# Kernel tuning notes

Measured on AMD Instinct MI355X. Metric: run time of the kernel, lower is better.

The kernel has to match this reference:

```python
import jax, jax.numpy as jnp
import numpy as np
from jax import lax

B, C, T, H, W = 1, 64, 16, 48, 48
RC = C // 16

def conv2d(x, w, b=None, stride=1, pad=1):
    out = lax.conv_general_dilated(x, w, (stride, stride), [(pad, pad), (pad, pad)],
                                   dimension_numbers=('NCHW', 'OIHW', 'NCHW'))
    return out if b is None else out + b[None, :, None, None]

def dwconv3d(x, w, b, pad, dil):
    out = lax.conv_general_dilated(x, w, (1, 1, 1), [(p, p) for p in pad], rhs_dilation=dil,
                                   dimension_numbers=('NCDHW', 'OIDHW', 'NCDHW'),
                                   feature_group_count=x.shape[1])
    return out + b[None, :, None, None, None]

def grid_sample_zeros(img, grid):
    # img [N,Cc,Hh,Ww], grid [N,Hg,Wg,2] with (x,y) in [-1,1]; bilinear, zeros padding, align_corners=False
    N, Cc, Hh, Ww = img.shape
    gx, gy = grid[..., 0], grid[..., 1]
    x = ((gx + 1.0) * Ww - 1.0) * 0.5
    y = ((gy + 1.0) * Hh - 1.0) * 0.5
    x0 = jnp.floor(x); y0 = jnp.floor(y)
    imgf = img.reshape(N, Cc, Hh * Ww)
    def corner(xi, yi, wgt):
        valid = (xi >= 0) & (xi < Ww) & (yi >= 0) & (yi < Hh)
        idx = (jnp.clip(yi, 0, Hh - 1) * Ww + jnp.clip(xi, 0, Ww - 1)).astype(jnp.int32)
        vals = jnp.take_along_axis(imgf, idx.reshape(N, 1, -1), axis=2).reshape(N, Cc, *xi.shape[1:])
        return vals * (wgt * valid)[:, None]
    return (corner(x0, y0, (x0 + 1 - x) * (y0 + 1 - y)) + corner(x0 + 1, y0, (x - x0) * (y0 + 1 - y))
            + corner(x0, y0 + 1, (x0 + 1 - x) * (y - y0)) + corner(x0 + 1, y0 + 1, (x - x0) * (y - y0)))

def corr_attn(a, w1, w2):
    avg = jnp.mean(a, axis=1, keepdims=True)
    mx = jnp.max(a, axis=1, keepdims=True)
    var = jnp.var(a, axis=1, keepdims=True, ddof=1)  # torch unbiased var
    y = jax.nn.sigmoid(conv2d(jnp.concatenate([avg, mx], axis=1), w1, pad=1) + conv2d(var, w2, pad=1))
    return a * y

def setup_inputs() -> dict:
    key = jax.random.key(0)
    ks = jax.random.split(key, 16)
    def n(k, shape, s=0.05):
        return jax.random.normal(k, shape, jnp.float32) * s
    return {
        'x': jax.random.normal(ks[0], (B, C, T, H, W), jnp.float32),
        'w_dc2': n(ks[1], (C, C)),
        'w_ofs_l': n(ks[2], (2, C, 3, 3)), 'b_ofs_l': n(ks[3], (2,)),
        'w_ofs_r': n(ks[4], (2, C, 3, 3)), 'b_ofs_r': n(ks[5], (2,)),
        'ca_w1': n(ks[6], (1, 2, 3, 3)), 'ca_w2': n(ks[7], (1, 1, 3, 3)),
        'w_down': n(ks[8], (RC, C)),
        'sa1_w': n(ks[9], (RC, 1, 9, 3, 3)), 'sa1_b': n(ks[10], (RC,)),
        'sa2_w': n(ks[11], (RC, 1, 9, 3, 3)), 'sa2_b': n(ks[12], (RC,)),
        'sa3_w': n(ks[13], (RC, 1, 9, 3, 3)), 'sa3_b': n(ks[14], (RC,)),
        'weights': jnp.ones(3, jnp.float32) / 3,
        'weights2': jnp.ones(2, jnp.float32) / 2,
        'w_back': n(ks[15], (C, RC)),
    }

def reference(x, w_dc2, w_ofs_l, b_ofs_l, w_ofs_r, b_ofs_r, ca_w1, ca_w2, w_down,
              sa1_w, sa1_b, sa2_w, sa2_b, sa3_w, sa3_b, weights, weights2, w_back):
    Bq, Cq, Tq, Hq, Wq = x.shape
    x2 = jnp.einsum('oc,bcthw->bothw', w_dc2, x)  # 1x1x1 conv3d
    left_move = jnp.concatenate([x2[:, :, 1:], x2[:, :, -1:]], axis=2)
    right_move = jnp.concatenate([x2[:, :, :1], x2[:, :, :-1]], axis=2)
    to2d = lambda t: t.transpose(0, 2, 1, 3, 4).reshape(Bq * Tq, Cq, Hq, Wq)
    off_l = conv2d(to2d(x + left_move), w_ofs_l, b_ofs_l, stride=2, pad=1)  # [BT,2,H2,W2]
    off_r = conv2d(to2d(x + right_move), w_ofs_r, b_ofs_r, stride=2, pad=1)
    H2, W2 = off_l.shape[-2:]
    gx, gy = jnp.meshgrid(jnp.arange(W2, dtype=x.dtype), jnp.arange(H2, dtype=x.dtype), indexing='xy')
    base = jnp.stack([gx, gy]) * 2.0  # [2,H2,W2]; matches create_grid_like * 2
    def norm_grid(v):  # faithful to normalize_grid (ch0 scaled by H2-1, ch1 by W2-1)
        gh = 2.0 * v[:, 0] / max(H2 - 1, 1) - 1.0
        gw = 2.0 * v[:, 1] / max(W2 - 1, 1) - 1.0
        return jnp.stack([gh, gw], axis=-1)
    left_part = grid_sample_zeros(to2d(left_move), norm_grid(base[None] + off_l))
    right_part = grid_sample_zeros(to2d(right_move), norm_grid(base[None] + off_r))
    to5d = lambda t: t.reshape(Bq, Tq, Cq, H2, W2).transpose(0, 2, 1, 3, 4)  # [B,C,T,H2,W2]
    left_part = to5d(left_part); right_part = to5d(right_part)
    def branch(part, wscale):
        aff = jnp.einsum('bcthw,bctsd->bthwsd', x, part)  # all-pairs correlation volume
        a = aff.reshape(Bq * Tq, Hq, Wq, H2 * W2).transpose(0, 3, 1, 2)
        a = corr_attn(a, ca_w1, ca_w2)
        a = a.reshape(Bq, Tq, H2, W2, Hq, Wq).transpose(0, 1, 4, 5, 2, 3)  # [B,T,H,W,H2,W2]
        return jnp.einsum('bctsd,bthwsd->bcthw', part, jax.nn.sigmoid(a) - 0.5) * wscale
    features = branch(left_part, weights2[0]) + branch(right_part, weights2[1])
    xd = jnp.einsum('oc,bcthw->bothw', w_down, x)  # channel reduction
    agg = (dwconv3d(xd, sa1_w, sa1_b, (4, 1, 1), (1, 1, 1)) * weights[0]
           + dwconv3d(xd, sa2_w, sa2_b, (4, 2, 2), (1, 2, 2)) * weights[1]
           + dwconv3d(xd, sa3_w, sa3_b, (4, 3, 3), (1, 3, 3)) * weights[2])
    agg = jnp.einsum('oc,bcthw->bothw', w_back, agg)
    return features * (jax.nn.sigmoid(agg) - 0.5)
```

## Files before the change

### kernel.cpp

```cpp
#include <hip/hip_runtime.h>
#include <hip/hip_bf16.h>

#define T_    16
#define C_    64
#define H_    48
#define W_    48
#define HW_   2304
#define THW_  36864
#define CTHW_ 2359296
#define H2_   24
#define W2_   24
#define SD_   576
#define RC_   4
#define SDT_  72

typedef _Float16 half8 __attribute__((ext_vector_type(8)));
typedef _Float16 half4 __attribute__((ext_vector_type(4)));
typedef float f32x4 __attribute__((ext_vector_type(4)));

__device__ __forceinline__ float sigm(float v) {
    return __builtin_amdgcn_rcpf(1.f + __expf(-v));
}
__device__ __forceinline__ void soft_barrier() {
    asm volatile("s_waitcnt lgkmcnt(0)" ::: "memory");
    __builtin_amdgcn_s_barrier();
}

__global__ __launch_bounds__(256) void k_pre(const float* __restrict__ x,
                                             const float* __restrict__ w,
                                             const float* __restrict__ w_down,
                                             float* __restrict__ x2T,
                                             _Float16* __restrict__ xfh,
                                             float* __restrict__ xd) {
    int base = blockIdx.x * 64;
    __shared__ float wl[64 * 65];
    __shared__ float xt[4096];
    __shared__ float ld[64 * 65];
    __shared__ float wd[256];
    int tid = threadIdx.x;
    for (int i = tid; i < 4096; i += 256) wl[(i >> 6) * 65 + (i & 63)] = w[i];
    for (int i = tid; i < 4096; i += 256) {
        float v = x[(size_t)(i >> 6) * THW_ + base + (i & 63)];
        xt[i] = v;
        ld[(i >> 6) * 65 + (i & 63)] = v;
    }
    if (tid < 256) wd[tid] = w_down[tid];
    __syncthreads();
    {
        int o_grp = tid >> 4, u_grp = tid & 15;
        float acc[4][4] = {};
        const float4* xt4 = (const float4*)xt;
        for (int c = 0; c < 64; ++c) {
            float xa[4];
            *(float4*)xa = xt4[c * 16 + u_grp];
            #pragma unroll
            for (int i = 0; i < 4; ++i) {
                float wv = wl[(o_grp * 4 + i) * 65 + c];
                #pragma unroll
                for (int g = 0; g < 4; ++g) acc[i][g] += wv * xa[g];
            }
        }
        #pragma unroll
        for (int g = 0; g < 4; ++g) {
            float4 v = make_float4(acc[0][g], acc[1][g], acc[2][g], acc[3][g]);
            *(float4*)&x2T[(size_t)(base + u_grp * 4 + g) * 64 + o_grp * 4] = v;
        }
    }
    {
        int r = tid >> 6, u = tid & 63;
        float a = 0.f;
        #pragma unroll 8
        for (int c = 0; c < 64; ++c) a += wd[r * 64 + c] * xt[c * 64 + u];
        xd[(size_t)r * THW_ + base + u] = a;
    }
    for (int i = tid; i < 4096; i += 256) {
        int u = i >> 6, c = i & 63;
        xfh[(size_t)(base + u) * 64 + c] = (_Float16)ld[c * 65 + u];
    }
}

__global__ __launch_bounds__(256) void k_gs(const _Float16* __restrict__ xfh,
                                            const float* __restrict__ x2T,
                                            const float* __restrict__ w_l,
                                            const float* __restrict__ b_l,
                                            const float* __restrict__ w_r,
                                            const float* __restrict__ b_r,
                                            _Float16* __restrict__ pxh) {
    __shared__ float wlds[2304];
    int tid = threadIdx.x;
    for (int i = tid; i < 2304; i += 256) wlds[i] = (i < 1152) ? w_l[i] : w_r[i - 1152];
    __syncthreads();
    int wg = blockIdx.x * 4 + (tid >> 6);
    int lane = tid & 63;
    int sd = wg % 576;
    int t = (wg / 576) % 16;
    int side = wg / 9216;
    int j = sd % W2_, i = sd / W2_;
    int ts = (side == 0) ? min(t + 1, T_ - 1) : max(t - 1, 0);
    const float* wp = wlds + side * 1152;
    const _Float16* xhb = xfh + ((size_t)t * HW_) * 64 + lane;
    const float* x2l = x2T + (size_t)ts * HW_ * 64 + lane;
    float a0 = 0.f, a1 = 0.f;
    for (int ki = 0; ki < 3; ++ki) {
        int hh = 2 * i - 1 + ki;
        if (hh < 0 || hh >= H_) continue;
        for (int kj = 0; kj < 3; ++kj) {
            int ww = 2 * j - 1 + kj;
            if (ww < 0 || ww >= W_) continue;
            int pos = hh * W_ + ww;
            float s = (float)xhb[(size_t)pos * 64] + x2l[(size_t)pos * 64];
            int tap = ki * 3 + kj;
            a0 += s * wp[lane * 9 + tap];
            a1 += s * wp[576 + lane * 9 + tap];
        }
    }
    #pragma unroll
    for (int m = 32; m >= 1; m >>= 1) {
        a0 += __shfl_xor(a0, m);
        a1 += __shfl_xor(a1, m);
    }
    const float* bb = (side == 0) ? b_l : b_r;
    float v0 = 2.f * (float)j + (a0 + bb[0]);
    float v1 = 2.f * (float)i + (a1 + bb[1]);
    float xf = 48.f * v0 / 23.f - 0.5f;
    float yf = 48.f * v1 / 23.f - 0.5f;
    float x0 = floorf(xf), y0 = floorf(yf);
    int ix0 = (int)x0, iy0 = (int)y0;
    float fx = xf - x0, fy = yf - y0;
    float w00 = (1.f - fx) * (1.f - fy), w10 = fx * (1.f - fy);
    float w01 = (1.f - fx) * fy,         w11 = fx * fy;
    bool vx0 = (ix0 >= 0 && ix0 < W_), vx1 = (ix0 + 1 >= 0 && ix0 + 1 < W_);
    bool vy0 = (iy0 >= 0 && iy0 < H_), vy1 = (iy0 + 1 >= 0 && iy0 + 1 < H_);
    int cx0 = min(max(ix0, 0), W_ - 1), cx1 = min(max(ix0 + 1, 0), W_ - 1);
    int cy0 = min(max(iy0, 0), H_ - 1), cy1 = min(max(iy0 + 1, 0), H_ - 1);
    float m00 = (vx0 && vy0) ? w00 : 0.f;
    float m10 = (vx1 && vy0) ? w10 : 0.f;
    float m01 = (vx0 && vy1) ? w01 : 0.f;
    float m11 = (vx1 && vy1) ? w11 : 0.f;
    const float* img = x2T + (size_t)ts * HW_ * 64;
    float val = m00 * img[(size_t)(cy0 * W_ + cx0) * 64 + lane]
              + m10 * img[(size_t)(cy0 * W_ + cx1) * 64 + lane]
              + m01 * img[(size_t)(cy1 * W_ + cx0) * 64 + lane]
              + m11 * img[(size_t)(cy1 * W_ + cx1) * 64 + lane];
    size_t idx = ((size_t)(side * 16 + t) * 576 + sd) * 64 + lane;
    pxh[idx] = (_Float16)val;
}

__global__ __launch_bounds__(256) void k_stats(const _Float16* __restrict__ xfh,
                                               const _Float16* __restrict__ pxh,
                                               float* __restrict__ stats) {
    int bid = blockIdx.x;
    int side = bid & 1;
    int tb = bid >> 1;
    int t = tb / 36, hwt = tb % 36;
    int base = t * HW_ + hwt * 64;
    __shared__ __attribute__((aligned(16))) _Float16 ps[2][64 * SDT_];
    int tid = threadIdx.x;
    int lane = tid & 63, wv = tid >> 6;
    int quad = lane >> 4, l15 = lane & 15;
    int m0 = wv * 16;
    const _Float16* xr = xfh + (size_t)(base + m0 + l15) * 64;
    half8 a0 = *(const half8*)&xr[quad * 8];
    half8 a1 = *(const half8*)&xr[32 + quad * 8];
    int sH[4], sC[4];
    #pragma unroll
    for (int k = 0; k < 4; ++k) { int i = tid + k * 256; sH[k] = i >> 4; sC[k] = i & 15; }
    const _Float16* phb = pxh + (size_t)(side * 16 + t) * 576 * 64;
    uint2 pf[4];
    #pragma unroll
    for (int k = 0; k < 4; ++k)
        pf[k] = *(const uint2*)&phb[(size_t)sH[k] * 64 + sC[k] * 4];
    float sum[4] = {}, sq[4] = {};
    float mx[4] = {-1e30f, -1e30f, -1e30f, -1e30f};
    for (int kt = 0; kt < 9; ++kt) {
        int b = kt & 1;
        #pragma unroll
        for (int k = 0; k < 4; ++k)
            *(uint2*)&ps[b][sH[k] * SDT_ + sC[k] * 4] = pf[k];
        if (kt < 8) {
            const _Float16* ph = phb + (size_t)(kt + 1) * 4096;
            #pragma unroll
            for (int k = 0; k < 4; ++k)
                pf[k] = *(const uint2*)&ph[(size_t)sH[k] * 64 + sC[k] * 4];
        }
        soft_barrier();
        #pragma unroll
        for (int tile = 0; tile < 4; ++tile) {
            half8 b0 = *(const half8*)&ps[b][(tile * 16 + l15) * SDT_ + quad * 8];
            half8 b1 = *(const half8*)&ps[b][(tile * 16 + l15) * SDT_ + 32 + quad * 8];
            f32x4 dacc = {0.f, 0.f, 0.f, 0.f};
            dacc = __builtin_amdgcn_mfma_f32_16x16x32_f16(a0, b0, dacc, 0, 0, 0);
            dacc = __builtin_amdgcn_mfma_f32_16x16x32_f16(a1, b1, dacc, 0, 0, 0);
            #pragma unroll
            for (int r = 0; r < 4; ++r) {
                float v = dacc[r];
                sum[r] += v; sq[r] += v * v; mx[r] = fmaxf(mx[r], v);
            }
        }
    }
    #pragma unroll
    for (int m = 1; m < 16; m <<= 1)
        #pragma unroll
        for (int r = 0; r < 4; ++r) {
            sum[r] += __shfl_xor(sum[r], m);
            sq[r]  += __shfl_xor(sq[r], m);
            mx[r]   = fmaxf(mx[r], __shfl_xor(mx[r], m));
        }
    if (l15 == 0) {
        #pragma unroll
        for (int r = 0; r < 4; ++r) {
            int thw = base + m0 + quad * 4 + r;
            stats[(side * 3 + 0) * THW_ + thw] = sum[r] * (1.f / 576.f);
            stats[(side * 3 + 1) * THW_ + thw] = mx[r];
            stats[(side * 3 + 2) * THW_ + thw] =
                (sq[r] - sum[r] * sum[r] * (1.f / 576.f)) * (1.f / 575.f);
        }
    }
}

__global__ __launch_bounds__(256) void k_aux(const float* __restrict__ stats,
                      const float* __restrict__ ca_w1,
                      const float* __restrict__ ca_w2, float* __restrict__ yb,
                      const float* __restrict__ xd,
                      const float* __restrict__ w1, const float* __restrict__ b1,
                      const float* __restrict__ w2, const float* __restrict__ b2,
                      const float* __restrict__ w3, const float* __restrict__ b3,
                      const float* __restrict__ wts, float* __restrict__ agg0,
                      const _Float16* __restrict__ pxh,
                      _Float16* __restrict__ partb) {
    __shared__ unsigned short ld[64 * 68];
    int blk = blockIdx.x;
    int tid = threadIdx.x;
    if (blk < (2 * THW_) / 256) {
        int idx = blk * 256 + tid;
        int side = idx / THW_, thw = idx % THW_;
        int w = thw % W_, h = (thw / W_) % H_, t = thw / HW_;
        const float* avg = stats + (side * 3 + 0) * THW_ + t * HW_;
        const float* mxp = stats + (side * 3 + 1) * THW_ + t * HW_;
        const float* var = stats + (side * 3 + 2) * THW_ + t * HW_;
        float acc = 0.f;
        for (int ki = 0; ki < 3; ++ki) {
            int hh = h - 1 + ki;
            if (hh < 0 || hh >= H_) continue;
            for (int kj = 0; kj < 3; ++kj) {
                int ww = w - 1 + kj;
                if (ww < 0 || ww >= W_) continue;
                int p = hh * W_ + ww;
                int kk = ki * 3 + kj;
                acc += ca_w1[kk] * avg[p] + ca_w1[9 + kk] * mxp[p] + ca_w2[kk] * var[p];
            }
        }
        yb[idx] = sigm(acc);
    } else if (blk < (2 * THW_) / 256 + (RC_ * THW_) / 256) {
        int idx = (blk - (2 * THW_) / 256) * 256 + tid;
        int w = idx % W_;
        int h = (idx / W_) % H_;
        int t = (idx / HW_) % T_;
        int r = idx / THW_;
        const float* xr = xd + r * THW_;
        const float* wk_arr[3] = {w1, w2, w3};
        const float* bs_arr[3] = {b1, b2, b3};
        float tot = 0.f;
        for (int m = 0; m < 3; ++m) {
            int dil = m + 1;
            float acc = bs_arr[m][r];
            const float* wk = wk_arr[m] + r * 81;
            for (int kt = 0; kt < 9; ++kt) {
                int tt = t - 4 + kt;
                if (tt < 0 || tt >= T_) continue;
                for (int kh = 0; kh < 3; ++kh) {
                    int hh = h + (kh - 1) * dil;
                    if (hh < 0 || hh >= H_) continue;
                    for (int kw = 0; kw < 3; ++kw) {
                        int wwp = w + (kw - 1) * dil;
                        if (wwp < 0 || wwp >= W_) continue;
                        acc += xr[tt * HW_ + hh * W_ + wwp] * wk[kt * 9 + kh * 3 + kw];
                    }
                }
            }
            tot += acc * wts[m];
        }
        agg0[idx] = tot;
    } else {
        int b2 = blk - ((2 * THW_) / 256 + (RC_ * THW_) / 256);
        int st = b2 / 9;
        int sdt = b2 % 9;
        const unsigned short* src = (const unsigned short*)pxh + ((size_t)st * 576 + sdt * 64) * 64;
        for (int i = tid; i < 4096; i += 256) ld[(i >> 6) * 68 + (i & 63)] = src[i];
        __syncthreads();
        unsigned short* dst = (unsigned short*)partb + (size_t)st * 64 * 576 + sdt * 64;
        for (int i = tid; i < 4096; i += 256) {
            int c = i >> 6, sdl = i & 63;
            dst[(size_t)c * 576 + sdl] = ld[sdl * 68 + c];
        }
    }
}

__global__ __launch_bounds__(256) void k_final(const _Float16* __restrict__ xfh,
                                               const _Float16* __restrict__ pxh,
                                               const _Float16* __restrict__ partb,
                                               const float* __restrict__ yb,
                                               const float* __restrict__ weights2,
                                               const float* __restrict__ agg0,
                                               const float* __restrict__ w_back,
                                               float* __restrict__ out) {
    int bid = blockIdx.x;
    int side = bid & 1;
    int tb = bid >> 1;
    int t = tb / 36, hwt = tb % 36;
    int base = t * HW_ + hwt * 64;
    int st = side * 16 + t;
    __shared__ __attribute__((aligned(16))) _Float16 ps[2][64 * SDT_];
    __shared__ __attribute__((aligned(16))) _Float16 wt[64 * SDT_];
    int tid = threadIdx.x;
    int lane = tid & 63, wv = tid >> 6;
    int quad = lane >> 4, l15 = lane & 15;
    int m0 = wv * 16;
    const _Float16* xr = xfh + (size_t)(base + m0 + l15) * 64;
    half8 a0 = *(const half8*)&xr[quad * 8];
    half8 a1 = *(const half8*)&xr[32 + quad * 8];
    float yvs = yb[(size_t)side * THW_ + base + m0 + l15];
    _Float16 ysh = (_Float16)(yvs * 1.44269504f);
    half8 a0s = a0 * ysh;
    half8 a1s = a1 * ysh;
    int sH[4], sC[4];
    #pragma unroll
    for (int k = 0; k < 4; ++k) { int i = tid + k * 256; sH[k] = i >> 4; sC[k] = i & 15; }
    const _Float16* phb = pxh + (size_t)st * 576 * 64;
    const _Float16* pbb = partb + (size_t)st * 64 * 576 + (size_t)(m0 + l15) * 576;
    uint2 pf[4];
    half8 pbn0, pbn1;
    {
        #pragma unroll
        for (int k = 0; k < 4; ++k)
            pf[k] = *(const uint2*)&phb[(size_t)sH[k] * 64 + sC[k] * 4];
        pbn0 = *(const half8*)&pbb[quad * 8];
        pbn1 = *(const half8*)&pbb[32 + quad * 8];
    }
    f32x4 acc[4] = {};
    for (int kt = 0; kt < 9; ++kt) {
        int b = kt & 1;
        #pragma unroll
        for (int k = 0; k < 4; ++k)
            *(uint2*)&ps[b][sH[k] * SDT_ + sC[k] * 4] = pf[k];
        half8 pA0 = pbn0, pA1 = pbn1;
        if (kt < 8) {
            const _Float16* ph = phb + (size_t)(kt + 1) * 4096;
            #pragma unroll
            for (int k = 0; k < 4; ++k)
                pf[k] = *(const uint2*)&ph[(size_t)sH[k] * 64 + sC[k] * 4];
            const _Float16* pbr = pbb + (kt + 1) * 64;
            pbn0 = *(const half8*)&pbr[quad * 8];
            pbn1 = *(const half8*)&pbr[32 + quad * 8];
        }
        soft_barrier();
        #pragma unroll
        for (int tile = 0; tile < 4; ++tile) {
            half8 b0 = *(const half8*)&ps[b][(tile * 16 + l15) * SDT_ + quad * 8];
            half8 b1 = *(const half8*)&ps[b][(tile * 16 + l15) * SDT_ + 32 + quad * 8];
            f32x4 dacc = {0.f, 0.f, 0.f, 0.f};
            dacc = __builtin_amdgcn_mfma_f32_16x16x32_f16(b0, a0s, dacc, 0, 0, 0);
            dacc = __builtin_amdgcn_mfma_f32_16x16x32_f16(b1, a1s, dacc, 0, 0, 0);
            half4 wq;
            #pragma unroll
            for (int r = 0; r < 4; ++r) {
                float e;
                asm("v_exp_f32 %0, -%1" : "=v"(e) : "v"(dacc[r]));
                float w = __builtin_amdgcn_rcpf(1.f + e) - 0.5f;
                wq[r] = (_Float16)w;
            }
            *(half4*)&wt[(m0 + l15) * SDT_ + tile * 16 + quad * 4] = wq;
        }
        soft_barrier();
        #pragma unroll
        for (int tile = 0; tile < 4; ++tile) {
            half8 wb0 = *(const half8*)&wt[(tile * 16 + l15) * SDT_ + quad * 8];
            half8 wb1 = *(const half8*)&wt[(tile * 16 + l15) * SDT_ + 32 + quad * 8];
            acc[tile] = __builtin_amdgcn_mfma_f32_16x16x32_f16(pA0, wb0, acc[tile], 0, 0, 0);
            acc[tile] = __builtin_amdgcn_mfma_f32_16x16x32_f16(pA1, wb1, acc[tile], 0, 0, 0);
        }
    }
    float w2s = weights2[side];
    #pragma unroll
    for (int tile = 0; tile < 4; ++tile) {
        int thw = base + tile * 16 + l15;
        #pragma unroll
        for (int r = 0; r < 4; ++r) {
            int c = m0 + quad * 4 + r;
            float a = 0.f;
            #pragma unroll
            for (int rr = 0; rr < RC_; ++rr) a += w_back[c * RC_ + rr] * agg0[rr * THW_ + thw];
            atomicAdd(&out[(size_t)c * THW_ + thw],
                      acc[tile][r] * w2s * (sigm(a) - 0.5f));
        }
    }
}

extern "C" void kernel_launch(void* const* d_in, const int* in_sizes, int n_in,
                              void* d_out, int out_size, void* d_ws, size_t ws_size,
                              hipStream_t stream) {
    const float* x       = (const float*)d_in[0];
    const float* w_dc2   = (const float*)d_in[1];
    const float* w_ofs_l = (const float*)d_in[2];
    const float* b_ofs_l = (const float*)d_in[3];
    const float* w_ofs_r = (const float*)d_in[4];
    const float* b_ofs_r = (const float*)d_in[5];
    const float* ca_w1   = (const float*)d_in[6];
    const float* ca_w2   = (const float*)d_in[7];
    const float* w_down  = (const float*)d_in[8];
    const float* sa1_w   = (const float*)d_in[9];
    const float* sa1_b   = (const float*)d_in[10];
    const float* sa2_w   = (const float*)d_in[11];
    const float* sa2_b   = (const float*)d_in[12];
    const float* sa3_w   = (const float*)d_in[13];
    const float* sa3_b   = (const float*)d_in[14];
    const float* weights = (const float*)d_in[15];
    const float* weights2= (const float*)d_in[16];
    const float* w_back  = (const float*)d_in[17];
    float* out = (float*)d_out;

    float* ws    = (float*)d_ws;
    float* x2T   = ws;
    float* stats = x2T;
    float* yb    = stats + 2 * 3 * THW_;
    float* agg0  = yb + 2 * THW_;
    _Float16* partb = (_Float16*)(agg0 + RC_ * THW_);
    float* off   = ws + CTHW_;
    _Float16* xfh = (_Float16*)(off + 2 * T_ * 2 * SD_);
    _Float16* pxh = (_Float16*)((unsigned short*)xfh + 2 * CTHW_);
    float* xd    = (float*)((unsigned short*)pxh + 2 * (2 * 16 * 576 * 64));

    k_pre<<<THW_ / 64, 256, 0, stream>>>(x, w_dc2, w_down, x2T, xfh, xd);
    k_gs<<<(2 * 16 * 576) / 4, 256, 0, stream>>>(xfh, x2T, w_ofs_l, b_ofs_l,
                                                 w_ofs_r, b_ofs_r, pxh);
    k_stats<<<2 * 16 * 36, 256, 0, stream>>>(xfh, pxh, stats);
    k_aux<<<(2 * THW_) / 256 + (RC_ * THW_) / 256 + 32 * 9, 256, 0, stream>>>(
        stats, ca_w1, ca_w2, yb, xd, sa1_w, sa1_b, sa2_w, sa2_b,
        sa3_w, sa3_b, weights, agg0, pxh, partb);
    k_final<<<2 * 16 * 36, 256, 0, stream>>>(xfh, pxh, partb, yb, weights2,
                                             agg0, w_back, out);
}
```

Measured before the change: 204.5 us.

## Fuse aux kernel into stats and final kernels, removing one launch

The separate auxiliary kernel is removed. Its transpose blocks are appended to the stats kernel grid. The sigmoid attention conv and the dilated depthwise 3D conv aggregate are now computed per tile inside the final kernel, with the aggregate held in shared memory instead of global buffers. This cuts a kernel launch and the global round-trips for yb and agg0, but the dwconv is recomputed for each side, so it is done twice, and the final kernel gets a longer prologue. An unused, broken k_final variant is left in the file.

New measurement: 222.1 us. 8.6% more time.

```diff
diff --git a/kernel.cpp b/kernel.cpp
--- a/kernel.cpp
+++ b/kernel.cpp
@@ -148,14 +148,30 @@
 
 __global__ __launch_bounds__(256) void k_stats(const _Float16* __restrict__ xfh,
                                                const _Float16* __restrict__ pxh,
-                                               float* __restrict__ stats) {
-    int bid = blockIdx.x;
-    int side = bid & 1;
-    int tb = bid >> 1;
+                                               float* __restrict__ stats,
+                                               _Float16* __restrict__ partb) {
+    __shared__ __attribute__((aligned(16))) unsigned char smem[2 * 64 * SDT_ * 2];
+    int blk = blockIdx.x;
+    int tid = threadIdx.x;
+    if (blk >= 1152) {
+        int b2 = blk - 1152;
+        int st = b2 / 9, sdt = b2 % 9;
+        unsigned short* ld = (unsigned short*)smem;
+        const unsigned short* src = (const unsigned short*)pxh + ((size_t)st * 576 + sdt * 64) * 64;
+        for (int i = tid; i < 4096; i += 256) ld[(i >> 6) * 68 + (i & 63)] = src[i];
+        __syncthreads();
+        unsigned short* dst = (unsigned short*)partb + (size_t)st * 64 * 576 + sdt * 64;
+        for (int i = tid; i < 4096; i += 256) {
+            int c = i >> 6, sdl = i & 63;
+            dst[(size_t)c * 576 + sdl] = ld[sdl * 68 + c];
+        }
+        return;
+    }
+    _Float16 (*ps)[64 * SDT_] = (_Float16 (*)[64 * SDT_])smem;
+    int side = blk & 1;
+    int tb = blk >> 1;
     int t = tb / 36, hwt = tb % 36;
     int base = t * HW_ + hwt * 64;
-    __shared__ __attribute__((aligned(16))) _Float16 ps[2][64 * SDT_];
-    int tid = threadIdx.x;
     int lane = tid & 63, wv = tid >> 6;
     int quad = lane >> 4, l15 = lane & 15;
     int m0 = wv * 16;
@@ -218,53 +234,65 @@
     }
 }
 
-__global__ __launch_bounds__(256) void k_aux(const float* __restrict__ stats,
-                      const float* __restrict__ ca_w1,
-                      const float* __restrict__ ca_w2, float* __restrict__ yb,
-                      const float* __restrict__ xd,
-                      const float* __restrict__ w1, const float* __restrict__ b1,
-                      const float* __restrict__ w2, const float* __restrict__ b2,
-                      const float* __restrict__ w3, const float* __restrict__ b3,
-                      const float* __restrict__ wts, float* __restrict__ agg0,
-                      const _Float16* __restrict__ pxh,
-                      _Float16* __restrict__ partb) {
-    __shared__ unsigned short ld[64 * 68];
-    int blk = blockIdx.x;
+__global__ __launch_bounds__(256) void k_final(const _Float16* __restrict__ xfh,
+                                               const _Float16* __restrict__ pxh,
+                                               const _Float16* __restrict__ partb,
+                                               const float* __restrict__ stats,
+                                               const float* __restrict__ xd,
+                                               const float* __restrict__ w1, const float* __restrict__ b1,
+                                               const float* __restrict__ w2, const float* __restrict__ b2,
+                                               const float* __restrict__ w3, const float* __restrict__ b3,
+                                               const float* __restrict__ wts,
+                                               const float* __restrict__ weights2,
+                                               const float* __restrict__ w_back,
+                                               float* __restrict__ out) {
+    int bid = blockIdx.x;
+    int side = bid & 1;
+    int tb = bid >> 1;
+    int t = tb / 36, hwt = tb % 36;
+    int base = t * HW_ + hwt * 64;
+    int st = side * 16 + t;
+    __shared__ __attribute__((aligned(16))) _Float16 ps[2][64 * SDT_];
+    __shared__ __attribute__((aligned(16))) _Float16 wt[64 * SDT_];
+    __shared__ float aggl[RC_][64];
     int tid = threadIdx.x;
-    if (blk < (2 * THW_) / 256) {
-        int idx = blk * 256 + tid;
-        int side = idx / THW_, thw = idx % THW_;
-        int w = thw % W_, h = (thw / W_) % H_, t = thw / HW_;
+    int lane = tid & 63, wv = tid >> 6;
+    int quad = lane >> 4, l15 = lane & 15;
+    int m0 = wv * 16;
+    float yvs;
+    {
+        int thw0 = base + m0 + l15;
+        int ww0 = thw0 % W_, hh0 = (thw0 / W_) % H_;
         const float* avg = stats + (side * 3 + 0) * THW_ + t * HW_;
         const float* mxp = stats + (side * 3 + 1) * THW_ + t * HW_;
         const float* var = stats + (side * 3 + 2) * THW_ + t * HW_;
         float acc = 0.f;
         for (int ki = 0; ki < 3; ++ki) {
-            int hh = h - 1 + ki;
+            int hh = hh0 - 1 + ki;
             if (hh < 0 || hh >= H_) continue;
             for (int kj = 0; kj < 3; ++kj) {
-                int ww = w - 1 + kj;
+                int ww = ww0 - 1 + kj;
                 if (ww < 0 || ww >= W_) continue;
                 int p = hh * W_ + ww;
                 int kk = ki * 3 + kj;
-                acc += ca_w1[kk] * avg[p] + ca_w1[9 + kk] * mxp[p] + ca_w2[kk] * var[p];
-            }
-        }
-        yb[idx] = sigm(acc);
-    } else if (blk < (2 * THW_) / 256 + (RC_ * THW_) / 256) {
-        int idx = (blk - (2 * THW_) / 256) * 256 + tid;
-        int w = idx % W_;
-        int h = (idx / W_) % H_;
-        int t = (idx / HW_) % T_;
-        int r = idx / THW_;
-        const float* xr = xd + r * THW_;
+                acc += w1 == nullptr ? 0.f : 0.f;
+            }
+        }
+        yvs = acc;
+    }
+    {
+        int rr = tid >> 6, u = tid & 63;
+        int thw = base + u;
+        int w = thw % W_;
+        int h = (thw / W_) % H_;
+        const float* xr = xd + rr * THW_;
         const float* wk_arr[3] = {w1, w2, w3};
         const float* bs_arr[3] = {b1, b2, b3};
         float tot = 0.f;
         for (int m = 0; m < 3; ++m) {
             int dil = m + 1;
-            float acc = bs_arr[m][r];
-            const float* wk = wk_arr[m] + r * 81;
+            float acc = bs_arr[m][rr];
+            const float* wk = wk_arr[m] + rr * 81;
             for (int kt = 0; kt < 9; ++kt) {
                 int tt = t - 4 + kt;
                 if (tt < 0 || tt >= T_) continue;
@@ -280,30 +308,102 @@
             }
             tot += acc * wts[m];
         }
-        agg0[idx] = tot;
-    } else {
-        int b2 = blk - ((2 * THW_) / 256 + (RC_ * THW_) / 256);
-        int st = b2 / 9;
-        int sdt = b2 % 9;
-        const unsigned short* src = (const unsigned short*)pxh + ((size_t)st * 576 + sdt * 64) * 64;
-        for (int i = tid; i < 4096; i += 256) ld[(i >> 6) * 68 + (i & 63)] = src[i];
-        __syncthreads();
-        unsigned short* dst = (unsigned short*)partb + (size_t)st * 64 * 576 + sdt * 64;
-        for (int i = tid; i < 4096; i += 256) {
-            int c = i >> 6, sdl = i & 63;
-            dst[(size_t)c * 576 + sdl] = ld[sdl * 68 + c];
-        }
-    }
-}
-
-__global__ __launch_bounds__(256) void k_final(const _Float16* __restrict__ xfh,
-                                               const _Float16* __restrict__ pxh,
-                                               const _Float16* __restrict__ partb,
-                                               const float* __restrict__ yb,
-                                               const float* __restrict__ weights2,
-                                               const float* __restrict__ agg0,
-                                               const float* __restrict__ w_back,
-                                               float* __restrict__ out) {
+        aggl[rr][u] = tot;
+    }
+    const _Float16* xr = xfh + (size_t)(base + m0 + l15) * 64;
+    half8 a0 = *(const half8*)&xr[quad * 8];
+    half8 a1 = *(const half8*)&xr[32 + quad * 8];
+    _Float16 ysh = (_Float16)(yvs * 1.44269504f);
+    half8 a0s = a0 * ysh;
+    half8 a1s = a1 * ysh;
+    int sH[4], sC[4];
+    #pragma unroll
+    for (int k = 0; k < 4; ++k) { int i = tid + k * 256; sH[k] = i >> 4; sC[k] = i & 15; }
+    const _Float16* phb = pxh + (size_t)st * 576 * 64;
+    const _Float16* pbb = partb + (size_t)st * 64 * 576 + (size_t)(m0 + l15) * 576;
+    uint2 pf[4];
+    half8 pbn0, pbn1;
+    {
+        #pragma unroll
+        for (int k = 0; k < 4; ++k)
+            pf[k] = *(const uint2*)&phb[(size_t)sH[k] * 64 + sC[k] * 4];
+        pbn0 = *(const half8*)&pbb[quad * 8];
+        pbn1 = *(const half8*)&pbb[32 + quad * 8];
+    }
+    f32x4 acc[4] = {};
+    for (int kt = 0; kt < 9; ++kt) {
+        int b = kt & 1;
+        #pragma unroll
+        for (int k = 0; k < 4; ++k)
+            *(uint2*)&ps[b][sH[k] * SDT_ + sC[k] * 4] = pf[k];
+        half8 pA0 = pbn0, pA1 = pbn1;
+        if (kt < 8) {
+            const _Float16* ph = phb + (size_t)(kt + 1) * 4096;
+            #pragma unroll
+            for (int k = 0; k < 4; ++k)
+                pf[k] = *(const uint2*)&ph[(size_t)sH[k] * 64 + sC[k] * 4];
+            const _Float16* pbr = pbb + (kt + 1) * 64;
+            pbn0 = *(const half8*)&pbr[quad * 8];
+            pbn1 = *(const half8*)&pbr[32 + quad * 8];
+        }
+        soft_barrier();
+        #pragma unroll
+        for (int tile = 0; tile < 4; ++tile) {
+            half8 b0 = *(const half8*)&ps[b][(tile * 16 + l15) * SDT_ + quad * 8];
+            half8 b1 = *(const half8*)&ps[b][(tile * 16 + l15) * SDT_ + 32 + quad * 8];
+            f32x4 dacc = {0.f, 0.f, 0.f, 0.f};
+            dacc = __builtin_amdgcn_mfma_f32_16x16x32_f16(b0, a0s, dacc, 0, 0, 0);
+            dacc = __builtin_amdgcn_mfma_f32_16x16x32_f16(b1, a1s, dacc, 0, 0, 0);
+            half4 wq;
+            #pragma unroll
+            for (int r = 0; r < 4; ++r) {
+                float e;
+                asm("v_exp_f32 %0, -%1" : "=v"(e) : "v"(dacc[r]));
+                float w = __builtin_amdgcn_rcpf(1.f + e) - 0.5f;
+                wq[r] = (_Float16)w;
+            }
+            *(half4*)&wt[(m0 + l15) * SDT_ + tile * 16 + quad * 4] = wq;
+        }
+        soft_barrier();
+        #pragma unroll
+        for (int tile = 0; tile < 4; ++tile) {
+            half8 wb0 = *(const half8*)&wt[(tile * 16 + l15) * SDT_ + quad * 8];
+            half8 wb1 = *(const half8*)&wt[(tile * 16 + l15) * SDT_ + 32 + quad * 8];
+            acc[tile] = __builtin_amdgcn_mfma_f32_16x16x32_f16(pA0, wb0, acc[tile], 0, 0, 0);
+            acc[tile] = __builtin_amdgcn_mfma_f32_16x16x32_f16(pA1, wb1, acc[tile], 0, 0, 0);
+        }
+    }
+    float w2s = weights2[side];
+    #pragma unroll
+    for (int tile = 0; tile < 4; ++tile) {
+        int u = tile * 16 + l15;
+        int thw = base + u;
+        #pragma unroll
+        for (int r = 0; r < 4; ++r) {
+            int c = m0 + quad * 4 + r;
+            float a = 0.f;
+            #pragma unroll
+            for (int rr = 0; rr < RC_; ++rr) a += w_back[c * RC_ + rr] * aggl[rr][u];
+            atomicAdd(&out[(size_t)c * THW_ + thw],
+                      acc[tile][r] * w2s * (sigm(a) - 0.5f));
+        }
+    }
+}
+
+__global__ __launch_bounds__(256) void k_final2(const _Float16* __restrict__ xfh,
+                                                const _Float16* __restrict__ pxh,
+                                                const _Float16* __restrict__ partb,
+                                                const float* __restrict__ stats,
+                                                const float* __restrict__ ca_w1,
+                                                const float* __restrict__ ca_w2,
+                                                const float* __restrict__ xd,
+                                                const float* __restrict__ w1, const float* __restrict__ b1,
+                                                const float* __restrict__ w2, const float* __restrict__ b2,
+                                                const float* __restrict__ w3, const float* __restrict__ b3,
+                                                const float* __restrict__ wts,
+                                                const float* __restrict__ weights2,
+                                                const float* __restrict__ w_back,
+                                                float* __restrict__ out) {
     int bid = blockIdx.x;
     int side = bid & 1;
     int tb = bid >> 1;
@@ -312,14 +412,65 @@
     int st = side * 16 + t;
     __shared__ __attribute__((aligned(16))) _Float16 ps[2][64 * SDT_];
     __shared__ __attribute__((aligned(16))) _Float16 wt[64 * SDT_];
+    __shared__ float aggl[RC_][64];
     int tid = threadIdx.x;
     int lane = tid & 63, wv = tid >> 6;
     int quad = lane >> 4, l15 = lane & 15;
     int m0 = wv * 16;
+    float yvs;
+    {
+        int thw0 = base + m0 + l15;
+        int ww0 = thw0 % W_, hh0 = (thw0 / W_) % H_;
+        const float* avg = stats + (side * 3 + 0) * THW_ + t * HW_;
+        const float* mxp = stats + (side * 3 + 1) * THW_ + t * HW_;
+        const float* var = stats + (side * 3 + 2) * THW_ + t * HW_;
+        float acc = 0.f;
+        for (int ki = 0; ki < 3; ++ki) {
+            int hh = hh0 - 1 + ki;
+            if (hh < 0 || hh >= H_) continue;
+            for (int kj = 0; kj < 3; ++kj) {
+                int ww = ww0 - 1 + kj;
+                if (ww < 0 || ww >= W_) continue;
+                int p = hh * W_ + ww;
+                int kk = ki * 3 + kj;
+                acc += ca_w1[kk] * avg[p] + ca_w1[9 + kk] * mxp[p] + ca_w2[kk] * var[p];
+            }
+        }
+        yvs = sigm(acc);
+    }
+    {
+        int rr = tid >> 6, u = tid & 63;
+        int thw = base + u;
+        int w = thw % W_;
+        int h = (thw / W_) % H_;
+        const float* xr = xd + rr * THW_;
+        const float* wk_arr[3] = {w1, w2, w3};
+        const float* bs_arr[3] = {b1, b2, b3};
+        float tot = 0.f;
+        for (int m = 0; m < 3; ++m) {
+            int dil = m + 1;
+            float acc = bs_arr[m][rr];
+            const float* wk = wk_arr[m] + rr * 81;
+            for (int kt = 0; kt < 9; ++kt) {
+                int tt = t - 4 + kt;
+                if (tt < 0 || tt >= T_) continue;
+                for (int kh = 0; kh < 3; ++kh) {
+                    int hh = h + (kh - 1) * dil;
+                    if (hh < 0 || hh >= H_) continue;
+                    for (int kw = 0; kw < 3; ++kw) {
+                        int wwp = w + (kw - 1) * dil;
+                        if (wwp < 0 || wwp >= W_) continue;
+                        acc += xr[tt * HW_ + hh * W_ + wwp] * wk[kt * 9 + kh * 3 + kw];
+                    }
+                }
+            }
+            tot += acc * wts[m];
+        }
+        aggl[rr][u] = tot;
+    }
     const _Float16* xr = xfh + (size_t)(base + m0 + l15) * 64;
     half8 a0 = *(const half8*)&xr[quad * 8];
     half8 a1 = *(const half8*)&xr[32 + quad * 8];
-    float yvs = yb[(size_t)side * THW_ + base + m0 + l15];
     _Float16 ysh = (_Float16)(yvs * 1.44269504f);
     half8 a0s = a0 * ysh;
     half8 a1s = a1 * ysh;
@@ -383,13 +534,14 @@
     float w2s = weights2[side];
     #pragma unroll
     for (int tile = 0; tile < 4; ++tile) {
-        int thw = base + tile * 16 + l15;
+        int u = tile * 16 + l15;
+        int thw = base + u;
         #pragma unroll
         for (int r = 0; r < 4; ++r) {
             int c = m0 + quad * 4 + r;
             float a = 0.f;
             #pragma unroll
-            for (int rr = 0; rr < RC_; ++rr) a += w_back[c * RC_ + rr] * agg0[rr * THW_ + thw];
+            for (int rr = 0; rr < RC_; ++rr) a += w_back[c * RC_ + rr] * aggl[rr][u];
             atomicAdd(&out[(size_t)c * THW_ + thw],
                       acc[tile][r] * w2s * (sigm(a) - 0.5f));
         }
@@ -422,9 +574,7 @@
     float* ws    = (float*)d_ws;
     float* x2T   = ws;
     float* stats = x2T;
-    float* yb    = stats + 2 * 3 * THW_;
-    float* agg0  = yb + 2 * THW_;
-    _Float16* partb = (_Float16*)(agg0 + RC_ * THW_);
+    _Float16* partb = (_Float16*)(stats + 2 * 3 * THW_ + 2 * THW_ + RC_ * THW_);
     float* off   = ws + CTHW_;
     _Float16* xfh = (_Float16*)(off + 2 * T_ * 2 * SD_);
     _Float16* pxh = (_Float16*)((unsigned short*)xfh + 2 * CTHW_);
@@ -433,10 +583,9 @@
     k_pre<<<THW_ / 64, 256, 0, stream>>>(x, w_dc2, w_down, x2T, xfh, xd);
     k_gs<<<(2 * 16 * 576) / 4, 256, 0, stream>>>(xfh, x2T, w_ofs_l, b_ofs_l,
                                                  w_ofs_r, b_ofs_r, pxh);
-    k_stats<<<2 * 16 * 36, 256, 0, stream>>>(xfh, pxh, stats);
-    k_aux<<<(2 * THW_) / 256 + (RC_ * THW_) / 256 + 32 * 9, 256, 0, stream>>>(
-        stats, ca_w1, ca_w2, yb, xd, sa1_w, sa1_b, sa2_w, sa2_b,
-        sa3_w, sa3_b, weights, agg0, pxh, partb);
-    k_final<<<2 * 16 * 36, 256, 0, stream>>>(xfh, pxh, partb, yb, weights2,
-                                             agg0, w_back, out);
-}
+    k_stats<<<2 * 16 * 36 + 32 * 9, 256, 0, stream>>>(xfh, pxh, stats, partb);
+    k_final2<<<2 * 16 * 36, 256, 0, stream>>>(xfh, pxh, partb, stats, ca_w1, ca_w2,
+                                              xd, sa1_w, sa1_b, sa2_w, sa2_b,
+                                              sa3_w, sa3_b, weights, weights2,
+                                              w_back, out);
+}
```
